# Performance work log

Hardware: AMD Instinct MI355X
Metric: run time of the kernel (lower is better)

The kernel has to match this reference:

```python
import jax, jax.numpy as jnp
import numpy as np

NUM_HEADS = 16


def _apply_rope(x, freqs):
    # x: (H, L, C), freqs: (L, C//2); computed in fp32, cast back to x.dtype
    xf = x.astype(jnp.float32)
    x1, x2 = jnp.split(xf, 2, axis=-1)
    f = freqs.astype(jnp.float32)[None]  # (1, L, C//2)
    cos, sin = jnp.cos(f), jnp.sin(f)
    out = jnp.concatenate((x1 * cos - x2 * sin, x1 * sin + x2 * cos), axis=-1)
    return out.astype(x.dtype)


def setup_inputs() -> dict:
    key = jax.random.key(0)
    k0, k1, k2, k3 = jax.random.split(key, 4)
    S, D, H = 4096, 1280, NUM_HEADS
    hd = D // H
    hidden_states = jax.random.normal(k0, (S, D), dtype=jnp.float32)
    cu_seqlens = jnp.array([0, 1024, 2048, 3072, 4096], dtype=jnp.int32)
    rotary_pos_emb = jax.random.normal(k1, (S, hd // 2), dtype=jnp.float32)
    scale = 1.0 / np.sqrt(D)
    w_qkv = (jax.random.normal(k2, (D, 3 * D), dtype=jnp.float32) * scale)
    b_qkv = jnp.zeros((3 * D,), dtype=jnp.float32)
    w_proj = (jax.random.normal(k3, (D, D), dtype=jnp.float32) * scale)
    b_proj = jnp.zeros((D,), dtype=jnp.float32)
    return {
        "hidden_states": hidden_states,
        "cu_seqlens": cu_seqlens,
        "rotary_pos_emb": rotary_pos_emb,
        "w_qkv": w_qkv,
        "b_qkv": b_qkv,
        "w_proj": w_proj,
        "b_proj": b_proj,
    }


def reference(hidden_states, cu_seqlens, rotary_pos_emb, w_qkv, b_qkv, w_proj, b_proj):
    S, D = hidden_states.shape
    H = NUM_HEADS
    hd = D // H
    qkv = hidden_states @ w_qkv + b_qkv            # (S, 3D)
    qkv = qkv.reshape(S, 3, H, hd).transpose(1, 2, 0, 3)  # (3, H, S, hd)
    q, k, v = qkv[0], qkv[1], qkv[2]
    q = _apply_rope(q, rotary_pos_emb)
    k = _apply_rope(k, rotary_pos_emb)
    # block-diagonal (per-segment) attention, equivalent to the per-segment loop
    seg = jnp.searchsorted(cu_seqlens, jnp.arange(S), side="right") - 1  # (S,)
    mask = seg[:, None] == seg[None, :]            # (S, S)
    scores = jnp.einsum("hqd,hkd->hqk", q, k) / np.sqrt(hd)
    scores = jnp.where(mask[None], scores, -jnp.inf)
    attn = jax.nn.softmax(scores.astype(jnp.float32), axis=-1).astype(q.dtype)
    out = jnp.einsum("hqk,hkd->qhd", attn, v).reshape(S, D)
    return out @ w_proj + b_proj
```

## Files before the change

kernel.cpp:

```cpp
#include <hip/hip_runtime.h>
#include <hip/hip_bf16.h>
#include <cstdint>

typedef __bf16 bf16x8 __attribute__((ext_vector_type(8)));
typedef __bf16 bf16x4 __attribute__((ext_vector_type(4)));
typedef short short4_ __attribute__((ext_vector_type(4)));
typedef float f32x4 __attribute__((ext_vector_type(4)));

#define SLEN 4096
#define DMODEL 1280
#define NHEADS 16
#define HD 80
#define HDP 96
#define KROW 104
#define VTILE_ELEMS 3328
#define VTILE_LDS 3584

#define GLD_LDS16(g, l)                                                        \
  __builtin_amdgcn_global_load_lds(                                            \
      (const __attribute__((address_space(1))) void*)(g),                      \
      (__attribute__((address_space(3))) void*)(l), 16, 0, 0)

#define WAIT_VMCNT(n) __builtin_amdgcn_s_waitcnt((n & 0xF) | 0x70 | 0xF00 | ((n >> 4) << 14))

__global__ __launch_bounds__(256) void cvt_f32_bf16(const float* __restrict__ in,
                                                    __bf16* __restrict__ out, int n4) {
  int i = blockIdx.x * 256 + threadIdx.x;
  if (i < n4) {
    float4 v = ((const float4*)in)[i];
    bf16x4 o = { (__bf16)v.x, (__bf16)v.y, (__bf16)v.z, (__bf16)v.w };
    ((bf16x4*)out)[i] = o;
  }
}

__global__ __launch_bounds__(256) void transpose_cvt(const float* __restrict__ in,
                                                     __bf16* __restrict__ out,
                                                     int K, int N) {
  __shared__ float tile[32][33];
  int n0 = blockIdx.x * 32, k0 = blockIdx.y * 32;
  int x = threadIdx.x & 31, y = threadIdx.x >> 5;
  for (int i = 0; i < 32; i += 8)
    tile[y + i][x] = in[(size_t)(k0 + y + i) * N + n0 + x];
  __syncthreads();
  for (int i = 0; i < 32; i += 8)
    out[(size_t)(n0 + y + i) * K + k0 + x] = (__bf16)tile[x][y + i];
}

__global__ __launch_bounds__(256) void gemm_bt(const __bf16* __restrict__ A,
                                               const __bf16* __restrict__ Bt,
                                               const float* __restrict__ bias,
                                               void* __restrict__ C,
                                               int M, int N, int K, int store_bf16) {
  __shared__ __attribute__((aligned(16))) __bf16 As[2][128 * 32];
  __shared__ __attribute__((aligned(16))) __bf16 Bs[2][128 * 32];
  const int t = threadIdx.x;
  const int lane = t & 63, wave = t >> 6;
  const int quad = lane >> 4, l15 = lane & 15;
  const int wm = (wave & 1) * 64, wn = (wave >> 1) * 64;
  const int bm = blockIdx.x * 128, bn = blockIdx.y * 128;

  const int r0s = (wave * 2) * 16 + (lane >> 2);
  const int cs = (lane & 3) * 8;
  const __bf16* Ag0 = A + (size_t)(bm + r0s) * K + cs;
  const __bf16* Ag1 = A + (size_t)(bm + r0s + 16) * K + cs;
  const __bf16* Bg0 = Bt + (size_t)(bn + r0s) * K + cs;
  const __bf16* Bg1 = Bt + (size_t)(bn + r0s + 16) * K + cs;
  const int ldso0 = (wave * 2) * 512;
  const int ldso1 = (wave * 2 + 1) * 512;

  f32x4 acc[4][4] = {};

  const int niter = K >> 5;

  GLD_LDS16(Ag0, &As[0][ldso0]);
  GLD_LDS16(Ag1, &As[0][ldso1]);
  GLD_LDS16(Bg0, &Bs[0][ldso0]);
  GLD_LDS16(Bg1, &Bs[0][ldso1]);

  for (int it = 0; it < niter; ++it) {
    const int cur = it & 1, nxt = cur ^ 1;
    const int kn = (it + 1) * 32;
    GLD_LDS16(Ag0 + kn, &As[nxt][ldso0]);
    GLD_LDS16(Ag1 + kn, &As[nxt][ldso1]);
    GLD_LDS16(Bg0 + kn, &Bs[nxt][ldso0]);
    GLD_LDS16(Bg1 + kn, &Bs[nxt][ldso1]);
    asm volatile("" ::: "memory");
    WAIT_VMCNT(4);
    __builtin_amdgcn_s_barrier();
    asm volatile("" ::: "memory");

    bf16x8 af[4], bfr[4];
#pragma unroll
    for (int i = 0; i < 4; ++i)
      af[i] = *(const bf16x8*)&As[cur][(wm + i * 16 + l15) * 32 + quad * 8];
#pragma unroll
    for (int j = 0; j < 4; ++j)
      bfr[j] = *(const bf16x8*)&Bs[cur][(wn + j * 16 + l15) * 32 + quad * 8];
#pragma unroll
    for (int i = 0; i < 4; ++i)
#pragma unroll
      for (int j = 0; j < 4; ++j)
        acc[i][j] = __builtin_amdgcn_mfma_f32_16x16x32_bf16(af[i], bfr[j], acc[i][j], 0, 0, 0);

    asm volatile("" ::: "memory");
    __builtin_amdgcn_s_barrier();
    asm volatile("" ::: "memory");
  }

  for (int j = 0; j < 4; ++j) {
    int col = bn + wn + j * 16 + l15;
    float bv = bias[col];
    for (int i = 0; i < 4; ++i) {
      int r0 = bm + wm + i * 16 + quad * 4;
      for (int r = 0; r < 4; ++r) {
        float v = acc[i][j][r] + bv;
        if (store_bf16)
          ((__bf16*)C)[(size_t)(r0 + r) * N + col] = (__bf16)v;
        else
          ((float*)C)[(size_t)(r0 + r) * N + col] = v;
      }
    }
  }
}

__global__ __launch_bounds__(256) void rope_pack(const __bf16* __restrict__ qkv,
                                                 const float* __restrict__ freqs,
                                                 __bf16* __restrict__ qp,
                                                 __bf16* __restrict__ kp,
                                                 __bf16* __restrict__ vt) {
  const float QSCALE = 0.11180339887498949f * 1.44269504088896340f;
  int h = blockIdx.y;
  int s0 = blockIdx.x * 64;
  int t = threadIdx.x;
  int sp = t >> 2, l4 = t & 3;
  int s = s0 + sp;
  const __bf16* row = qkv + (size_t)s * 3840 + h * 80;
  __bf16* qo = qp + (size_t)(h * SLEN + s) * HDP;
  __bf16* ko = kp + (size_t)(h * SLEN + s) * KROW;

#pragma unroll
  for (int k = 0; k < 10; ++k) {
    int j = l4 * 10 + k;
    float f = freqs[s * 40 + j];
    float cs = __builtin_cosf(f), sn = __builtin_sinf(f);
    float x1 = (float)row[j], x2 = (float)row[j + 40];
    float y1 = (float)row[1280 + j], y2 = (float)row[1280 + j + 40];
    qo[j]      = (__bf16)((x1 * cs - x2 * sn) * QSCALE);
    qo[j + 40] = (__bf16)((x1 * sn + x2 * cs) * QSCALE);
    ko[j]      = (__bf16)(y1 * cs - y2 * sn);
    ko[j + 40] = (__bf16)(y1 * sn + y2 * cs);
  }
#pragma unroll
  for (int k = 0; k < 4; ++k) {
    int c = 80 + l4 * 4 + k;
    qo[c] = (__bf16)0.f;
    ko[c] = (__bf16)0.f;
  }

  __shared__ float vtile[64][81];
#pragma unroll
  for (int k = 0; k < 20; ++k) {
    int d = l4 * 20 + k;
    vtile[sp][d] = (float)row[2560 + d];
  }
  __syncthreads();
  int key = t & 31, g8 = t >> 5;
  for (int c2 = 0; c2 < 2; ++c2) {
    __bf16* tb = vt + (size_t)(h * (SLEN / 32) + (s0 >> 5) + c2) * VTILE_ELEMS;
#pragma unroll
    for (int k = 0; k < 10; ++k) {
      int d = g8 * 10 + k;
      tb[d * 40 + key] = (__bf16)vtile[c2 * 32 + key][d];
    }
  }
}

__global__ __launch_bounds__(256) void flash_attn(const __bf16* __restrict__ qp,
                                                  const __bf16* __restrict__ kp,
                                                  const __bf16* __restrict__ vt,
                                                  const int* __restrict__ cu, int nseg,
                                                  __bf16* __restrict__ out) {
  const float MEXP = 16.0f;
  int h = blockIdx.y;
  int q0 = blockIdx.x * 64;
  int seg = 0;
  for (int i = 1; i < nseg; ++i)
    if (cu[i] <= q0) seg = i;
  int kstart = cu[seg], kend = cu[seg + 1];

  int t = threadIdx.x;
  int lane = t & 63, wave = t >> 6;
  int quad = lane >> 4, l15 = lane & 15;

  __shared__ __attribute__((aligned(16))) __bf16 Ks[64 * KROW];
  __shared__ __attribute__((aligned(16))) __bf16 Vs[2 * VTILE_LDS];

  bf16x8 qf[3];
  {
    const __bf16* qptr = qp + (size_t)(h * SLEN + q0 + wave * 16 + l15) * HDP + quad * 8;
    qf[0] = *(const bf16x8*)(qptr);
    qf[1] = *(const bf16x8*)(qptr + 32);
    qf[2] = *(const bf16x8*)(qptr + 64);
  }

  f32x4 o[5] = {};
  float l_p = 0.f;

  const __bf16* gK = kp + (size_t)(h * SLEN + kstart) * KROW + lane * 8;
  const __bf16* gV = vt + (size_t)(h * (SLEN / 32) + (kstart >> 5)) * VTILE_ELEMS + lane * 8;

  int niter = (kend - kstart) >> 6;

  for (int it = 0; it < niter; ++it) {
    __syncthreads();
    for (int i = wave; i < 13; i += 4)
      GLD_LDS16(gK + i * 512, &Ks[i * 512]);
    for (int i = wave; i < 7; i += 4)
      GLD_LDS16(gV + i * 512, &Vs[i * 512]);
    for (int i = wave; i < 7; i += 4)
      GLD_LDS16(gV + VTILE_ELEMS + i * 512, &Vs[VTILE_LDS + i * 512]);
    gK += 64 * KROW;
    gV += 2 * VTILE_ELEMS;
    __syncthreads();

    f32x4 sc[4];
#pragma unroll
    for (int nt = 0; nt < 4; ++nt) {
      sc[nt] = f32x4{-MEXP, -MEXP, -MEXP, -MEXP};
#pragma unroll
      for (int c = 0; c < 3; ++c) {
        bf16x8 kf = *(const bf16x8*)&Ks[(nt * 16 + l15) * KROW + quad * 8 + c * 32];
        sc[nt] = __builtin_amdgcn_mfma_f32_16x16x32_bf16(kf, qf[c], sc[nt], 0, 0, 0);
      }
    }

    bf16x4 pf[4];
#pragma unroll
    for (int nt = 0; nt < 4; ++nt)
#pragma unroll
      for (int r = 0; r < 4; ++r) {
        float p = __builtin_amdgcn_exp2f(sc[nt][r]);
        l_p += p;
        pf[nt][r] = (__bf16)p;
      }

#pragma unroll
    for (int kq = 0; kq < 4; ++kq) {
      int vbase = (kq >> 1) * VTILE_LDS + (kq & 1) * 16 + quad * 4;
#pragma unroll
      for (int dt = 0; dt < 5; ++dt) {
        bf16x4 vfr = *(const bf16x4*)&Vs[vbase + (dt * 16 + l15) * 40];
        o[dt] = __builtin_amdgcn_mfma_f32_16x16x16bf16_1k(
            *(short4_*)&vfr, *(short4_*)&pf[kq], o[dt], 0, 0, 0);
      }
    }
  }

  l_p += __shfl_xor(l_p, 16);
  l_p += __shfl_xor(l_p, 32);
  float rinv = 1.0f / l_p;

  int qrow = q0 + wave * 16 + l15;
#pragma unroll
  for (int dt = 0; dt < 5; ++dt) {
    bf16x4 ov;
#pragma unroll
    for (int r = 0; r < 4; ++r)
      ov[r] = (__bf16)(o[dt][r] * rinv);
    *(bf16x4*)&out[(size_t)qrow * DMODEL + h * 80 + dt * 16 + quad * 4] = ov;
  }
}

extern "C" void kernel_launch(void* const* d_in, const int* in_sizes, int n_in,
                              void* d_out, int out_size, void* d_ws, size_t ws_size,
                              hipStream_t stream) {
  const float* hidden = (const float*)d_in[0];
  const int* cu       = (const int*)d_in[1];
  const float* freqs  = (const float*)d_in[2];
  const float* w_qkv  = (const float*)d_in[3];
  const float* b_qkv  = (const float*)d_in[4];
  const float* w_proj = (const float*)d_in[5];
  const float* b_proj = (const float*)d_in[6];
  float* out = (float*)d_out;

  char* ws = (char*)d_ws;
  size_t off = 0;
  auto alloc = [&](size_t bytes) {
    char* p = ws + off;
    off += (bytes + 255) & ~(size_t)255;
    return p;
  };
  __bf16* hid_b  = (__bf16*)alloc((size_t)SLEN * DMODEL * 2);
  __bf16* wqkvT  = (__bf16*)alloc((size_t)3840 * 1280 * 2);
  __bf16* wprojT = (__bf16*)alloc((size_t)1280 * 1280 * 2);
  __bf16* qkvb   = (__bf16*)alloc((size_t)SLEN * 3840 * 2);
  __bf16* qp     = (__bf16*)alloc((size_t)NHEADS * SLEN * HDP * 2);
  __bf16* kp     = (__bf16*)alloc((size_t)NHEADS * SLEN * KROW * 2 + 1024);
  __bf16* vt     = (__bf16*)alloc((size_t)NHEADS * (SLEN / 32) * VTILE_ELEMS * 2 + 1024);
  __bf16* attn   = hid_b;

  cvt_f32_bf16<<<(SLEN * DMODEL / 4 + 255) / 256, 256, 0, stream>>>(hidden, hid_b, SLEN * DMODEL / 4);
  transpose_cvt<<<dim3(3840 / 32, 1280 / 32), 256, 0, stream>>>(w_qkv, wqkvT, 1280, 3840);
  transpose_cvt<<<dim3(1280 / 32, 1280 / 32), 256, 0, stream>>>(w_proj, wprojT, 1280, 1280);
  gemm_bt<<<dim3(SLEN / 128, 3840 / 128), 256, 0, stream>>>(hid_b, wqkvT, b_qkv, qkvb,
                                                            SLEN, 3840, 1280, 1);
  rope_pack<<<dim3(SLEN / 64, NHEADS), 256, 0, stream>>>(qkvb, freqs, qp, kp, vt);
  int nseg = in_sizes[1] - 1;
  flash_attn<<<dim3(SLEN / 64, NHEADS), 256, 0, stream>>>(qp, kp, vt, cu, nseg, attn);
  gemm_bt<<<dim3(SLEN / 128, DMODEL / 128), 256, 0, stream>>>(attn, wprojT, b_proj, out,
                                                              SLEN, DMODEL, 1280, 0);
}
```

Before: 266.9 us.

## Triple-buffer GEMM loads and widen QKV GEMM tile to 256 rows

The bf16 GEMM kernel is templated on the number of M-waves. Its LDS staging goes from double to triple buffering with a two-iteration prefetch distance, so global-to-LDS loads have more time to land before the barrier. The QKV projection now uses 256x128 tiles with 512 threads, so each B tile is loaded once for twice as many rows. The output projection keeps 128x128 tiles. The costs are more LDS per block, which may lower occupancy, and fewer blocks for the QKV GEMM (480 instead of 960).

```diff
diff --git a/kernel.cpp b/kernel.cpp
--- a/kernel.cpp
+++ b/kernel.cpp
@@ -46,56 +46,74 @@
     out[(size_t)(n0 + y + i) * K + k0 + x] = (__bf16)tile[x][y + i];
 }
 
-__global__ __launch_bounds__(256) void gemm_bt(const __bf16* __restrict__ A,
-                                               const __bf16* __restrict__ Bt,
-                                               const float* __restrict__ bias,
-                                               void* __restrict__ C,
-                                               int M, int N, int K, int store_bf16) {
-  __shared__ __attribute__((aligned(16))) __bf16 As[2][128 * 32];
-  __shared__ __attribute__((aligned(16))) __bf16 Bs[2][128 * 32];
+template <int WMW>
+__global__ __launch_bounds__(WMW * 2 * 64) void gemm_bt(const __bf16* __restrict__ A,
+                                                        const __bf16* __restrict__ Bt,
+                                                        const float* __restrict__ bias,
+                                                        void* __restrict__ C,
+                                                        int M, int N, int K, int store_bf16) {
+  constexpr int BM = WMW * 64;
+  constexpr int NW = WMW * 2;
+  constexpr int BI = 8 / NW;
+  constexpr int PW = 2 + BI;
+  constexpr int ASZ = BM * 32, BSZ = 128 * 32;
+
+  __shared__ __attribute__((aligned(16))) __bf16 As[3][ASZ];
+  __shared__ __attribute__((aligned(16))) __bf16 Bs[3][BSZ];
+
   const int t = threadIdx.x;
   const int lane = t & 63, wave = t >> 6;
   const int quad = lane >> 4, l15 = lane & 15;
-  const int wm = (wave & 1) * 64, wn = (wave >> 1) * 64;
-  const int bm = blockIdx.x * 128, bn = blockIdx.y * 128;
-
-  const int r0s = (wave * 2) * 16 + (lane >> 2);
-  const int cs = (lane & 3) * 8;
-  const __bf16* Ag0 = A + (size_t)(bm + r0s) * K + cs;
-  const __bf16* Ag1 = A + (size_t)(bm + r0s + 16) * K + cs;
-  const __bf16* Bg0 = Bt + (size_t)(bn + r0s) * K + cs;
-  const __bf16* Bg1 = Bt + (size_t)(bn + r0s + 16) * K + cs;
-  const int ldso0 = (wave * 2) * 512;
-  const int ldso1 = (wave * 2 + 1) * 512;
+  const int wm = (wave & (WMW - 1)) * 64, wn = (wave / WMW) * 64;
+  const int bm = blockIdx.x * BM, bn = blockIdx.y * 128;
+
+  const int rs = lane >> 2, cs = (lane & 3) * 8;
+  const __bf16* AgQ[2];
+  const __bf16* BgQ[BI];
+  int aLds[2], bLds[BI];
+#pragma unroll
+  for (int q = 0; q < 2; ++q) {
+    int row = (wave * 2 + q) * 16;
+    AgQ[q] = A + (size_t)(bm + row + rs) * K + cs;
+    aLds[q] = row * 32;
+  }
+#pragma unroll
+  for (int q = 0; q < BI; ++q) {
+    int row = (wave * BI + q) * 16;
+    BgQ[q] = Bt + (size_t)(bn + row + rs) * K + cs;
+    bLds[q] = row * 32;
+  }
 
   f32x4 acc[4][4] = {};
-
   const int niter = K >> 5;
 
-  GLD_LDS16(Ag0, &As[0][ldso0]);
-  GLD_LDS16(Ag1, &As[0][ldso1]);
-  GLD_LDS16(Bg0, &Bs[0][ldso0]);
-  GLD_LDS16(Bg1, &Bs[0][ldso1]);
-
+#pragma unroll
+  for (int s = 0; s < 2; ++s) {
+#pragma unroll
+    for (int q = 0; q < 2; ++q) GLD_LDS16(AgQ[q] + s * 32, &As[s][aLds[q]]);
+#pragma unroll
+    for (int q = 0; q < BI; ++q) GLD_LDS16(BgQ[q] + s * 32, &Bs[s][bLds[q]]);
+  }
+
+  int cmp = 0, stg = 2;
   for (int it = 0; it < niter; ++it) {
-    const int cur = it & 1, nxt = cur ^ 1;
-    const int kn = (it + 1) * 32;
-    GLD_LDS16(Ag0 + kn, &As[nxt][ldso0]);
-    GLD_LDS16(Ag1 + kn, &As[nxt][ldso1]);
-    GLD_LDS16(Bg0 + kn, &Bs[nxt][ldso0]);
-    GLD_LDS16(Bg1 + kn, &Bs[nxt][ldso1]);
+    const int kk = (it + 2 < niter ? it + 2 : niter - 1) * 32;
+#pragma unroll
+    for (int q = 0; q < 2; ++q) GLD_LDS16(AgQ[q] + kk, &As[stg][aLds[q]]);
+#pragma unroll
+    for (int q = 0; q < BI; ++q) GLD_LDS16(BgQ[q] + kk, &Bs[stg][bLds[q]]);
     asm volatile("" ::: "memory");
-    WAIT_VMCNT(4);
+    WAIT_VMCNT(2 * PW);
     __builtin_amdgcn_s_barrier();
     asm volatile("" ::: "memory");
 
     bf16x8 af[4], bfr[4];
 #pragma unroll
     for (int i = 0; i < 4; ++i)
-      af[i] = *(const bf16x8*)&As[cur][(wm + i * 16 + l15) * 32 + quad * 8];
+      af[i] = *(const bf16x8*)&As[cmp][(wm + i * 16 + l15) * 32 + quad * 8];
 #pragma unroll
     for (int j = 0; j < 4; ++j)
-      bfr[j] = *(const bf16x8*)&Bs[cur][(wn + j * 16 + l15) * 32 + quad * 8];
+      bfr[j] = *(const bf16x8*)&Bs[cmp][(wn + j * 16 + l15) * 32 + quad * 8];
 #pragma unroll
     for (int i = 0; i < 4; ++i)
 #pragma unroll
@@ -105,6 +123,8 @@
     asm volatile("" ::: "memory");
     __builtin_amdgcn_s_barrier();
     asm volatile("" ::: "memory");
+    cmp = (cmp == 2) ? 0 : cmp + 1;
+    stg = (stg == 2) ? 0 : stg + 1;
   }
 
   for (int j = 0; j < 4; ++j) {
@@ -302,11 +322,11 @@
   cvt_f32_bf16<<<(SLEN * DMODEL / 4 + 255) / 256, 256, 0, stream>>>(hidden, hid_b, SLEN * DMODEL / 4);
   transpose_cvt<<<dim3(3840 / 32, 1280 / 32), 256, 0, stream>>>(w_qkv, wqkvT, 1280, 3840);
   transpose_cvt<<<dim3(1280 / 32, 1280 / 32), 256, 0, stream>>>(w_proj, wprojT, 1280, 1280);
-  gemm_bt<<<dim3(SLEN / 128, 3840 / 128), 256, 0, stream>>>(hid_b, wqkvT, b_qkv, qkvb,
-                                                            SLEN, 3840, 1280, 1);
+  gemm_bt<4><<<dim3(SLEN / 256, 3840 / 128), 512, 0, stream>>>(hid_b, wqkvT, b_qkv, qkvb,
+                                                               SLEN, 3840, 1280, 1);
   rope_pack<<<dim3(SLEN / 64, NHEADS), 256, 0, stream>>>(qkvb, freqs, qp, kp, vt);
   int nseg = in_sizes[1] - 1;
   flash_attn<<<dim3(SLEN / 64, NHEADS), 256, 0, stream>>>(qp, kp, vt, cu, nseg, attn);
-  gemm_bt<<<dim3(SLEN / 128, DMODEL / 128), 256, 0, stream>>>(attn, wprojT, b_proj, out,
-                                                              SLEN, DMODEL, 1280, 0);
-}
+  gemm_bt<2><<<dim3(SLEN / 128, DMODEL / 128), 256, 0, stream>>>(attn, wprojT, b_proj, out,
+                                                                 SLEN, DMODEL, 1280, 0);
+}
```

New measurement: 251.7 us. 5.7% less time.
